# Kernel optimization log

Hardware: AMD Instinct MI355X
Metric: run time of the kernel (lower is better)

## Reference

```python
import jax, jax.numpy as jnp
import numpy as np

N_NODES = 100000
N_EDGES = 300000
D_IN = 256
D_OUT = 256


def setup_inputs() -> dict:
    key = jax.random.key(0)
    k1, k2, k3 = jax.random.split(key, 3)
    z = jax.random.normal(k1, (N_NODES, D_IN), dtype=jnp.float32)
    edge_index = jax.random.randint(k2, (2, N_EDGES), 0, N_NODES, dtype=jnp.int64)
    # Linear(input_dim, out_dim): weight [out, in], stored transposed for x @ W
    W = jax.random.normal(k3, (D_IN, D_OUT), dtype=jnp.float32) / np.sqrt(D_IN)
    b = jnp.zeros((D_OUT,), dtype=jnp.float32)
    return {"z": z, "edge_index": edge_index, "W": W, "b": b}


def reference(z, edge_index, W, b):
    # h = Linear(z): [N, D_out]
    h = z @ W + b
    # gather endpoint embeddings and take per-edge dot product
    src = h[edge_index[0]]  # [E, D_out]
    dst = h[edge_index[1]]  # [E, D_out]
    value = jnp.sum(src * dst, axis=1)  # [E]
    return jax.nn.sigmoid(value)
```

## Files before the change

kernel.cpp:

```cpp
#include <hip/hip_runtime.h>
#include <hip/hip_bf16.h>
#include <hip/hip_fp16.h>
#include <math.h>


#define D_DIM 256
#define BM 64

typedef __attribute__((ext_vector_type(8))) short bf16x8;
typedef __attribute__((ext_vector_type(4))) float f32x4;

__device__ bf16x8 g_Wh[8 * 256 * 4];
__device__ bf16x8 g_Wl[8 * 256 * 4];

__device__ inline unsigned short bf16_rn(float x) {
  unsigned u = __builtin_bit_cast(unsigned, x);
  unsigned r = u + 0x7FFFu + ((u >> 16) & 1u);
  return (unsigned short)(r >> 16);
}
__device__ inline float bf16_f(unsigned short s) {
  return __builtin_bit_cast(float, (unsigned)s << 16);
}

__device__ inline void split8_rne(const float4 f0, const float4 f1, bf16x8& hi, bf16x8& lo) {
  float v[8] = {f0.x, f0.y, f0.z, f0.w, f1.x, f1.y, f1.z, f1.w};
#pragma unroll
  for (int j = 0; j < 8; j++) {
    unsigned short hb = bf16_rn(v[j]);
    hi[j] = (short)hb;
    lo[j] = (short)bf16_rn(v[j] - bf16_f(hb));
  }
}

__device__ inline void split8_trunc(const float4 f0, const float4 f1, bf16x8& hi, bf16x8& lo) {
  unsigned u[8];
  u[0] = __builtin_bit_cast(unsigned, f0.x); u[1] = __builtin_bit_cast(unsigned, f0.y);
  u[2] = __builtin_bit_cast(unsigned, f0.z); u[3] = __builtin_bit_cast(unsigned, f0.w);
  u[4] = __builtin_bit_cast(unsigned, f1.x); u[5] = __builtin_bit_cast(unsigned, f1.y);
  u[6] = __builtin_bit_cast(unsigned, f1.z); u[7] = __builtin_bit_cast(unsigned, f1.w);
  unsigned* hp = (unsigned*)&hi;
  unsigned* lp = (unsigned*)&lo;
#pragma unroll
  for (int p = 0; p < 4; p++) {
    unsigned a = u[2 * p], c = u[2 * p + 1];
    hp[p] = (a >> 16) | (c & 0xFFFF0000u);
    float la = __builtin_bit_cast(float, a) - __builtin_bit_cast(float, a & 0xFFFF0000u);
    float lc = __builtin_bit_cast(float, c) - __builtin_bit_cast(float, c & 0xFFFF0000u);
    lp[p] = (__builtin_bit_cast(unsigned, la) >> 16) |
            (__builtin_bit_cast(unsigned, lc) & 0xFFFF0000u);
  }
}

__global__ __launch_bounds__(256) void pack_w_kernel(const float* __restrict__ W) {
  int t = blockIdx.x * 256 + threadIdx.x;
  int kb = t >> 10;
  int qd = (t >> 8) & 3;
  int n  = t & 255;
  float v[8];
#pragma unroll
  for (int j = 0; j < 8; j++)
    v[j] = W[(size_t)(kb * 32 + qd * 8 + j) * D_DIM + n];
  bf16x8 hi, lo;
  split8_rne(make_float4(v[0], v[1], v[2], v[3]),
             make_float4(v[4], v[5], v[6], v[7]), hi, lo);
  int fi = (kb * 256 + n) * 4 + qd;
  g_Wh[fi] = hi;
  g_Wl[fi] = lo;
}

__device__ inline void stage_b(int kb, char* buf, int wv, int lane) {
  const char* gsrc = (wv < 4)
      ? ((const char*)g_Wh + (size_t)kb * 16384 + (wv & 3) * 4096)
      : ((const char*)g_Wl + (size_t)kb * 16384 + (wv & 3) * 4096);
  char* ldst = buf + ((wv < 4) ? 0 : 16384) + (wv & 3) * 4096;
#pragma unroll
  for (int i = 0; i < 4; i++) {
    __builtin_amdgcn_global_load_lds(
        (const __attribute__((address_space(1))) void*)(gsrc + i * 1024 + lane * 16),
        (__attribute__((address_space(3))) void*)(ldst + i * 1024),
        16, 0, 0);
  }
}

__global__ __launch_bounds__(512) void gemm_mfma_kernel(
    const float* __restrict__ z, const float* __restrict__ b,
    __half* __restrict__ h, int nrows) {
  __shared__ char smem[34816];
  const int tid = threadIdx.x;
  const int lane = tid & 63;
  const int wv = tid >> 6;
  const int mf = wv >> 1;
  const int nh = wv & 1;
  const int fr = lane & 15;
  const int qd = lane >> 4;
  const int row0 = blockIdx.x * BM + mf * 16;

  f32x4 acc[8];
#pragma unroll
  for (int j = 0; j < 8; j++) acc[j] = (f32x4)0.f;

  int ar = row0 + fr;
  ar = ar < nrows ? ar : (nrows - 1);
  const float* zrow = z + (size_t)ar * D_DIM + qd * 8;

  float4 a0 = *(const float4*)(zrow);
  float4 a1 = *(const float4*)(zrow + 4);

#pragma unroll 1
  for (int kb = 0; kb < 8; kb++) {
    __syncthreads();
    stage_b(kb, smem, wv, lane);
    bf16x8 ah, al;
    split8_trunc(a0, a1, ah, al);
    __syncthreads();
    if (kb < 7) {
      const float* p = zrow + (kb + 1) * 32;
      a0 = *(const float4*)(p);
      a1 = *(const float4*)(p + 4);
    }
    const bf16x8* bufh = (const bf16x8*)smem;
    const bf16x8* bufl = (const bf16x8*)(smem + 16384);
#pragma unroll
    for (int fn = 0; fn < 8; fn++) {
      int fi = (nh * 128 + fn * 16 + fr) * 4 + qd;
      bf16x8 bh = bufh[fi];
      bf16x8 bl = bufl[fi];
      acc[fn] = __builtin_amdgcn_mfma_f32_16x16x32_bf16(ah, bh, acc[fn], 0, 0, 0);
      acc[fn] = __builtin_amdgcn_mfma_f32_16x16x32_bf16(ah, bl, acc[fn], 0, 0, 0);
      acc[fn] = __builtin_amdgcn_mfma_f32_16x16x32_bf16(al, bh, acc[fn], 0, 0, 0);
    }
  }
  __syncthreads();

  __half* et = (__half*)(smem + wv * 4352);
  float bias[8];
#pragma unroll
  for (int fn = 0; fn < 8; fn++) bias[fn] = b[nh * 128 + fn * 16 + fr];

#pragma unroll
  for (int fn = 0; fn < 8; fn++)
#pragma unroll
    for (int r = 0; r < 4; r++)
      et[(qd * 4 + r) * 136 + fn * 16 + fr] = __float2half(acc[fn][r] + bias[fn]);
#pragma unroll
  for (int p = 0; p < 4; p++) {
    int idx = p * 64 + lane;
    int rr = idx >> 4;
    int cc = idx & 15;
    float4 v = *(const float4*)(et + rr * 136 + cc * 8);
    int row = row0 + rr;
    if (row < nrows)
      *(float4*)(h + (size_t)row * D_DIM + nh * 128 + cc * 8) = v;
  }
}

__global__ __launch_bounds__(256) void edge_dot_kernel(
    const int* __restrict__ ei, const __half* __restrict__ h,
    float* __restrict__ out, int E) {
  int wid = (blockIdx.x * blockDim.x + threadIdx.x) >> 6;
  int lane = threadIdx.x & 63;
  int ebase = wid * 8;
  if (ebase >= E) return;
  const int half = lane >> 5;
  const int off = lane & 31;

  float4 v[8];
#pragma unroll
  for (int q = 0; q < 8; q++) {
    int e = ebase + q;
    e = e < E ? e : (E - 1);
    int node = half ? ei[E + e] : ei[e];
    v[q] = *(const float4*)((const __half*)h + (size_t)node * D_DIM + off * 8);
  }

  float res = 0.f;
#pragma unroll
  for (int q = 0; q < 8; q++) {
    float4 w;
    w.x = __shfl_xor(v[q].x, 32);
    w.y = __shfl_xor(v[q].y, 32);
    w.z = __shfl_xor(v[q].z, 32);
    w.w = __shfl_xor(v[q].w, 32);
    const __half2* a2 = (const __half2*)&v[q];
    const __half2* b2 = (const __half2*)&w;
    float part = 0.f;
#pragma unroll
    for (int j = 0; j < 4; j++) {
      float2 fa = __half22float2(a2[j]);
      float2 fb = __half22float2(b2[j]);
      part += fa.x * fb.x + fa.y * fb.y;
    }
#pragma unroll
    for (int m = 1; m <= 16; m <<= 1) part += __shfl_xor(part, m);
    res = (lane == q) ? part : res;
  }
  if (lane < 8) {
    int e = ebase + lane;
    if (e < E) out[e] = 1.0f / (1.0f + __expf(-res));
  }
}

extern "C" void kernel_launch(void* const* d_in, const int* in_sizes, int n_in,
                              void* d_out, int out_size, void* d_ws, size_t ws_size,
                              hipStream_t stream) {
  const float* z  = (const float*)d_in[0];
  const int*   ei = (const int*)d_in[1];
  const float* W  = (const float*)d_in[2];
  const float* b  = (const float*)d_in[3];
  float* out = (float*)d_out;
  __half* h  = (__half*)d_ws;

  const int nnodes = in_sizes[0] / D_DIM;
  const int E = in_sizes[1] / 2;

  pack_w_kernel<<<32, 256, 0, stream>>>(W);

  dim3 grid_gemm((nnodes + BM - 1) / BM);
  gemm_mfma_kernel<<<grid_gemm, 512, 0, stream>>>(z, b, h, nnodes);

  int waves = (E + 7) / 8;
  dim3 grid_edge(((size_t)waves * 64 + 255) / 256);
  edge_dot_kernel<<<grid_edge, 256, 0, stream>>>(ei, h, out, E);
}
```

Before: 230.7 us.

## Replace split-bf16 triple MFMA with single fp16 MFMA and double-buffer W tiles

Drops the bf16 hi/lo split of both z and W, which needed three MFMAs per fragment, and instead converts both to fp16 and issues one f16 MFMA per fragment. W is packed once as fp16, halving staging traffic. Tiles are now double-buffered in LDS so the next tile's global-to-LDS load overlaps the current compute, with one barrier per iteration. This reduces GEMM precision to fp16 inputs, which risks accuracy loss or overflow for large values.

```diff
diff --git a/kernel.cpp b/kernel.cpp
--- a/kernel.cpp
+++ b/kernel.cpp
@@ -7,74 +7,28 @@
 #define D_DIM 256
 #define BM 64
 
-typedef __attribute__((ext_vector_type(8))) short bf16x8;
+typedef __attribute__((ext_vector_type(8))) _Float16 half8;
 typedef __attribute__((ext_vector_type(4))) float f32x4;
 
-__device__ bf16x8 g_Wh[8 * 256 * 4];
-__device__ bf16x8 g_Wl[8 * 256 * 4];
-
-__device__ inline unsigned short bf16_rn(float x) {
-  unsigned u = __builtin_bit_cast(unsigned, x);
-  unsigned r = u + 0x7FFFu + ((u >> 16) & 1u);
-  return (unsigned short)(r >> 16);
-}
-__device__ inline float bf16_f(unsigned short s) {
-  return __builtin_bit_cast(float, (unsigned)s << 16);
-}
-
-__device__ inline void split8_rne(const float4 f0, const float4 f1, bf16x8& hi, bf16x8& lo) {
-  float v[8] = {f0.x, f0.y, f0.z, f0.w, f1.x, f1.y, f1.z, f1.w};
-#pragma unroll
-  for (int j = 0; j < 8; j++) {
-    unsigned short hb = bf16_rn(v[j]);
-    hi[j] = (short)hb;
-    lo[j] = (short)bf16_rn(v[j] - bf16_f(hb));
-  }
-}
-
-__device__ inline void split8_trunc(const float4 f0, const float4 f1, bf16x8& hi, bf16x8& lo) {
-  unsigned u[8];
-  u[0] = __builtin_bit_cast(unsigned, f0.x); u[1] = __builtin_bit_cast(unsigned, f0.y);
-  u[2] = __builtin_bit_cast(unsigned, f0.z); u[3] = __builtin_bit_cast(unsigned, f0.w);
-  u[4] = __builtin_bit_cast(unsigned, f1.x); u[5] = __builtin_bit_cast(unsigned, f1.y);
-  u[6] = __builtin_bit_cast(unsigned, f1.z); u[7] = __builtin_bit_cast(unsigned, f1.w);
-  unsigned* hp = (unsigned*)&hi;
-  unsigned* lp = (unsigned*)&lo;
-#pragma unroll
-  for (int p = 0; p < 4; p++) {
-    unsigned a = u[2 * p], c = u[2 * p + 1];
-    hp[p] = (a >> 16) | (c & 0xFFFF0000u);
-    float la = __builtin_bit_cast(float, a) - __builtin_bit_cast(float, a & 0xFFFF0000u);
-    float lc = __builtin_bit_cast(float, c) - __builtin_bit_cast(float, c & 0xFFFF0000u);
-    lp[p] = (__builtin_bit_cast(unsigned, la) >> 16) |
-            (__builtin_bit_cast(unsigned, lc) & 0xFFFF0000u);
-  }
-}
+__device__ half8 g_Wf[8 * 256 * 4];
 
 __global__ __launch_bounds__(256) void pack_w_kernel(const float* __restrict__ W) {
   int t = blockIdx.x * 256 + threadIdx.x;
   int kb = t >> 10;
   int qd = (t >> 8) & 3;
   int n  = t & 255;
-  float v[8];
+  half8 o;
 #pragma unroll
   for (int j = 0; j < 8; j++)
-    v[j] = W[(size_t)(kb * 32 + qd * 8 + j) * D_DIM + n];
-  bf16x8 hi, lo;
-  split8_rne(make_float4(v[0], v[1], v[2], v[3]),
-             make_float4(v[4], v[5], v[6], v[7]), hi, lo);
-  int fi = (kb * 256 + n) * 4 + qd;
-  g_Wh[fi] = hi;
-  g_Wl[fi] = lo;
+    o[j] = (_Float16)W[(size_t)(kb * 32 + qd * 8 + j) * D_DIM + n];
+  g_Wf[(kb * 256 + n) * 4 + qd] = o;
 }
 
 __device__ inline void stage_b(int kb, char* buf, int wv, int lane) {
-  const char* gsrc = (wv < 4)
-      ? ((const char*)g_Wh + (size_t)kb * 16384 + (wv & 3) * 4096)
-      : ((const char*)g_Wl + (size_t)kb * 16384 + (wv & 3) * 4096);
-  char* ldst = buf + ((wv < 4) ? 0 : 16384) + (wv & 3) * 4096;
+  const char* gsrc = (const char*)g_Wf + (size_t)kb * 16384 + wv * 2048;
+  char* ldst = buf + wv * 2048;
 #pragma unroll
-  for (int i = 0; i < 4; i++) {
+  for (int i = 0; i < 2; i++) {
     __builtin_amdgcn_global_load_lds(
         (const __attribute__((address_space(1))) void*)(gsrc + i * 1024 + lane * 16),
         (__attribute__((address_space(3))) void*)(ldst + i * 1024),
@@ -105,32 +59,34 @@
 
   float4 a0 = *(const float4*)(zrow);
   float4 a1 = *(const float4*)(zrow + 4);
+  stage_b(0, smem, wv, lane);
+  __syncthreads();
 
 #pragma unroll 1
   for (int kb = 0; kb < 8; kb++) {
-    __syncthreads();
-    stage_b(kb, smem, wv, lane);
-    bf16x8 ah, al;
-    split8_trunc(a0, a1, ah, al);
-    __syncthreads();
+    char* cur = smem + (kb & 1) * 16384;
+    if (kb < 7) stage_b(kb + 1, smem + ((kb + 1) & 1) * 16384, wv, lane);
+
+    half8 af;
+    af[0] = (_Float16)a0.x; af[1] = (_Float16)a0.y;
+    af[2] = (_Float16)a0.z; af[3] = (_Float16)a0.w;
+    af[4] = (_Float16)a1.x; af[5] = (_Float16)a1.y;
+    af[6] = (_Float16)a1.z; af[7] = (_Float16)a1.w;
     if (kb < 7) {
       const float* p = zrow + (kb + 1) * 32;
       a0 = *(const float4*)(p);
       a1 = *(const float4*)(p + 4);
     }
-    const bf16x8* bufh = (const bf16x8*)smem;
-    const bf16x8* bufl = (const bf16x8*)(smem + 16384);
+
+    const half8* buf = (const half8*)cur;
 #pragma unroll
     for (int fn = 0; fn < 8; fn++) {
       int fi = (nh * 128 + fn * 16 + fr) * 4 + qd;
-      bf16x8 bh = bufh[fi];
-      bf16x8 bl = bufl[fi];
-      acc[fn] = __builtin_amdgcn_mfma_f32_16x16x32_bf16(ah, bh, acc[fn], 0, 0, 0);
-      acc[fn] = __builtin_amdgcn_mfma_f32_16x16x32_bf16(ah, bl, acc[fn], 0, 0, 0);
-      acc[fn] = __builtin_amdgcn_mfma_f32_16x16x32_bf16(al, bh, acc[fn], 0, 0, 0);
+      half8 bf = buf[fi];
+      acc[fn] = __builtin_amdgcn_mfma_f32_16x16x32_f16(af, bf, acc[fn], 0, 0, 0);
     }
+    __syncthreads();
   }
-  __syncthreads();
 
   __half* et = (__half*)(smem + wv * 4352);
   float bias[8];
```

Result: faster. 218.0 us (-5.5%).
